# Performance work log

Measured on AMD Instinct MI355X. Metric: run time of the kernel, lower is better.

The kernel has to match this reference:

```python
import jax, jax.numpy as jnp
from jax import lax
import numpy as np

N, L = 32, 2048
TABLES, INPUT_SIZE, DEM_IN, DEM_OUT = 4, 1024, 8, 20
C_TAB = INPUT_SIZE // TABLES  # 256
LIN_IN = INPUT_SIZE + DEM_OUT  # 1044
EPS = 1e-5


def _layernorm(x):
    # LNNormalizer modeled as affine-free LayerNorm over last dim
    mu = jnp.mean(x, axis=-1, keepdims=True)
    var = jnp.mean(jnp.square(x - mu), axis=-1, keepdims=True)
    return (x - mu) * lax.rsqrt(var + EPS)


def setup_inputs() -> dict:
    key = jax.random.key(0)
    ks = jax.random.split(key, 11)
    inp = {
        "dem": jax.random.normal(ks[0], (N, DEM_IN), jnp.float32),
        "ts0": jax.random.normal(ks[1], (N, L, C_TAB), jnp.float32),
        "ts1": jax.random.normal(ks[2], (N, L, C_TAB), jnp.float32),
        "ts2": jax.random.normal(ks[3], (N, L, C_TAB), jnp.float32),
        "ts3": jax.random.normal(ks[4], (N, L, C_TAB), jnp.float32),
        "W_dem1": jax.random.normal(ks[5], (DEM_IN, 40), jnp.float32) * (1.0 / np.sqrt(DEM_IN)),
        "b_dem1": jnp.zeros((40,), jnp.float32),
        "W_dem2": jax.random.normal(ks[6], (40, DEM_OUT), jnp.float32) * (1.0 / np.sqrt(40.0)),
        "b_dem2": jnp.zeros((DEM_OUT,), jnp.float32),
        "W_lin": jax.random.normal(ks[7], (LIN_IN, C_TAB), jnp.float32) * (1.0 / np.sqrt(LIN_IN)),
        "b_lin": jnp.zeros((C_TAB,), jnp.float32),
    }
    return inp


def reference(dem, ts0, ts1, ts2, ts3, W_dem1, b_dem1, W_dem2, b_dem2, W_lin, b_lin):
    # dem_fc: 8 -> 40 -> 20 with ReLUs (dropout=0)
    d = jax.nn.relu(dem @ W_dem1 + b_dem1)
    d = jax.nn.relu(d @ W_dem2 + b_dem2)                 # [N, 20]
    dem_exp = jnp.broadcast_to(d[:, None, :], (N, L, DEM_OUT))

    x = jnp.concatenate([ts0, ts1, ts2, ts3, dem_exp], axis=-1)  # [N, L, 1044]
    x = x @ W_lin + b_lin                                        # [N, L, 256]

    t = jnp.arange(L, dtype=jnp.int32)[None, :, None]            # [1, L, 1]
    pad_mask = t < (L - 1)  # positions whose causal window includes zero padding

    # --- causal max pool (= cummax, with padding zeros in window) + argmax ---
    idx = jnp.broadcast_to(t, x.shape).astype(jnp.int32)

    def comb(a, b):
        va, ia = a
        vb, ib = b
        keep = va >= vb  # first-occurrence tie-break, like torch max_pool1d
        return jnp.where(keep, va, vb), jnp.where(keep, ia, ib)

    cmax, carg = lax.associative_scan(comb, (x, idx), axis=1)
    p_max = jnp.where(pad_mask, jnp.maximum(cmax, 0.0), cmax)    # [N, L, 256]
    # torch index into padded buffer minus (L-1): padding zero (at window start,
    time_inds = jnp.where(pad_mask & (cmax <= 0.0), t - (L - 1), carg)

    # --- causal avg pool: window always L, zeros counted (count_include_pad) ---
    csum = jnp.cumsum(x, axis=1)
    p_avg = csum / jnp.float32(L)

    # --- norm_sum_pool1d: causal sum normalized by sqrt(#valid elements) ---
    p_sum = csum * lax.rsqrt((t + 1).astype(jnp.float32))

    activations = jnp.swapaxes(p_max, 1, 2)      # [N, C, L], pre-normalization
    time_inds_out = jnp.swapaxes(time_inds, 1, 2)

    p_max = _layernorm(p_max)
    p_avg = _layernorm(p_avg)
    p_sum = _layernorm(p_sum)

    out = jnp.concatenate([p_max, p_avg, p_sum, dem_exp], axis=-1)  # [N, L, 788]
    return out, time_inds_out, activations
```

## Files before the change

kernel.cpp:

```cpp
#include <hip/hip_runtime.h>

#define NBATCH 32
#define LSEQ   2048
#define CDIM   256
#define KDIM   1024
#define DEMI   8
#define H1DIM  40
#define DEMO   20
#define NCHUNK 32
#define CHLEN  64
#define LNEPS  1e-5f

#define OFF_X    0L
#define OFF_S    16777216L
#define OFF_AGM  33554432L
#define OFF_AGS  33816576L
#define OFF_AGI  34078720L
#define OFF_PRM  34340864L
#define OFF_PRS  34603008L
#define OFF_PRI  34865152L
#define OFF_DV   35127296L
#define OFF_BASE 35127936L

#define OUT0_OFF   0L
#define OUTTI_OFF  51642368L
#define OUTACT_OFF 68419584L

typedef short          s16x8 __attribute__((ext_vector_type(8)));
typedef unsigned short us4   __attribute__((ext_vector_type(4)));
typedef float          f32x4 __attribute__((ext_vector_type(4)));

static __device__ __forceinline__ unsigned short f2bf(float x) {
    unsigned u = __builtin_bit_cast(unsigned, x);
    u += 0x7fffu + ((u >> 16) & 1u);
    return (unsigned short)(u >> 16);
}
static __device__ __forceinline__ float bf2f(unsigned short h) {
    return __builtin_bit_cast(float, ((unsigned)h) << 16);
}

__global__ __launch_bounds__(256) void k_dem(
    const float* __restrict__ dem,
    const float* __restrict__ W1, const float* __restrict__ b1,
    const float* __restrict__ W2, const float* __restrict__ b2,
    const float* __restrict__ Wl, const float* __restrict__ bl,
    float* __restrict__ dvals, float* __restrict__ base)
{
    __shared__ float h1[NBATCH][H1DIM];
    __shared__ float dsh[NBATCH][DEMO];
    int tid = threadIdx.x;

    for (int idx = tid; idx < NBATCH * H1DIM; idx += 256) {
        int n = idx / H1DIM, o = idx % H1DIM;
        float s = b1[o];
        #pragma unroll
        for (int k = 0; k < DEMI; ++k) s += dem[n * DEMI + k] * W1[k * H1DIM + o];
        h1[n][o] = fmaxf(s, 0.0f);
    }
    __syncthreads();
    for (int idx = tid; idx < NBATCH * DEMO; idx += 256) {
        int n = idx / DEMO, o = idx % DEMO;
        float s = b2[o];
        #pragma unroll
        for (int k = 0; k < H1DIM; ++k) s += h1[n][k] * W2[k * DEMO + o];
        float dv = fmaxf(s, 0.0f);
        dsh[n][o] = dv;
        dvals[idx] = dv;
    }
    __syncthreads();
    for (int idx = tid; idx < NBATCH * CDIM; idx += 256) {
        int n = idx >> 8, c = idx & 255;
        float s = bl[c];
        #pragma unroll
        for (int k = 0; k < DEMO; ++k) s += dsh[n][k] * Wl[(KDIM + k) * CDIM + c];
        base[idx] = s;
    }
}

__global__ __launch_bounds__(256) void k_wconv(
    const float* __restrict__ W, unsigned short* __restrict__ Wf)
{
    int idx = blockIdx.x * 256 + threadIdx.x;
    int k = idx >> 8, c = idx & 255;
    float w = W[idx];
    unsigned short h = f2bf(w);
    float r1 = w - bf2f(h);
    unsigned short m = f2bf(r1);
    float r2 = r1 - bf2f(m);
    unsigned short l = f2bf(r2);
    int kstep = k >> 5;
    int nt = c >> 4;
    int ln = (c & 15) + (((k & 31) >> 3) << 4);
    int e = k & 7;
    long o = (((long)(kstep * 3) * 16 + nt) * 64 + ln) * 8 + e;
    Wf[o]         = h;
    Wf[o + 8192]  = m;
    Wf[o + 16384] = l;
}

__global__ __launch_bounds__(256) void k_gemm(
    const float* __restrict__ ts0, const float* __restrict__ ts1,
    const float* __restrict__ ts2, const float* __restrict__ ts3,
    const unsigned short* __restrict__ Wf, const float* __restrict__ base,
    float* __restrict__ X)
{
    __shared__ unsigned short Af[3][8][64][8];
    __shared__ unsigned short Bf[3][8][64][8];

    const int tid  = threadIdx.x;
    const int lane = tid & 63;
    const int wid  = tid >> 6;

    const int mb = blockIdx.x >> 1;
    const int cb = (blockIdx.x & 1) << 7;
    const int n  = mb >> 4;
    const int t0 = (mb & 15) << 7;

    const int kq  = tid & 1;
    const int am  = tid >> 1;
    const int amt = am >> 4, aml = am & 15;
    const long arow = ((long)(n * LSEQ + t0 + am)) * CDIM;

    f32x4 acc[4][4];
    #pragma unroll
    for (int i = 0; i < 4; ++i)
        #pragma unroll
        for (int j = 0; j < 4; ++j)
            #pragma unroll
            for (int r = 0; r < 4; ++r) acc[i][j][r] = 0.0f;

    const uint4* wsrc = (const uint4*)Wf;
    uint4* bdst = (uint4*)(&Bf[0][0][0][0]);

    for (int k0 = 0; k0 < KDIM; k0 += 32) {
        const float* tsp = (k0 < 256) ? ts0 : (k0 < 512) ? ts1 : (k0 < 768) ? ts2 : ts3;
        const int joff = k0 & 255;

        float4 av[4];
        #pragma unroll
        for (int j = 0; j < 4; ++j)
            av[j] = *(const float4*)(tsp + arow + joff + kq * 4 + j * 8);

        const int kstep = k0 >> 5;
        const long wbase = (long)kstep * 3072 + ((cb >> 4) << 6);
        uint4 bv[6];
        #pragma unroll
        for (int p = 0; p < 3; ++p) {
            bv[p * 2 + 0] = wsrc[wbase + p * 1024 + tid];
            bv[p * 2 + 1] = wsrc[wbase + p * 1024 + tid + 256];
        }

        __syncthreads();

        #pragma unroll
        for (int j = 0; j < 4; ++j) {
            const float vv[4] = {av[j].x, av[j].y, av[j].z, av[j].w};
            us4 hv, mv, lv;
            #pragma unroll
            for (int q = 0; q < 4; ++q) {
                float v = vv[q];
                unsigned short h = f2bf(v);
                float r1 = v - bf2f(h);
                unsigned short m = f2bf(r1);
                float r2 = r1 - bf2f(m);
                unsigned short l = f2bf(r2);
                hv[q] = h; mv[q] = m; lv[q] = l;
            }
            const int ln = aml + (j << 4);
            const int e0 = kq << 2;
            *(us4*)&Af[0][amt][ln][e0] = hv;
            *(us4*)&Af[1][amt][ln][e0] = mv;
            *(us4*)&Af[2][amt][ln][e0] = lv;
        }
        #pragma unroll
        for (int p = 0; p < 3; ++p) {
            bdst[p * 512 + tid]       = bv[p * 2 + 0];
            bdst[p * 512 + tid + 256] = bv[p * 2 + 1];
        }

        __syncthreads();

        const int wmt = (wid >> 1) << 2;
        const int wnt = (wid & 1) << 2;
        s16x8 ah[4], am2[4], al2[4];
        #pragma unroll
        for (int mt = 0; mt < 4; ++mt) {
            ah[mt]  = *(const s16x8*)&Af[0][wmt + mt][lane][0];
            am2[mt] = *(const s16x8*)&Af[1][wmt + mt][lane][0];
            al2[mt] = *(const s16x8*)&Af[2][wmt + mt][lane][0];
        }
        #pragma unroll
        for (int nt = 0; nt < 4; ++nt) {
            s16x8 bh = *(const s16x8*)&Bf[0][wnt + nt][lane][0];
            s16x8 bm = *(const s16x8*)&Bf[1][wnt + nt][lane][0];
            s16x8 bl = *(const s16x8*)&Bf[2][wnt + nt][lane][0];
            #pragma unroll
            for (int mt = 0; mt < 4; ++mt) {
                acc[mt][nt] = __builtin_amdgcn_mfma_f32_16x16x32_bf16(ah[mt],  bl, acc[mt][nt], 0, 0, 0);
                acc[mt][nt] = __builtin_amdgcn_mfma_f32_16x16x32_bf16(al2[mt], bh, acc[mt][nt], 0, 0, 0);
                acc[mt][nt] = __builtin_amdgcn_mfma_f32_16x16x32_bf16(am2[mt], bm, acc[mt][nt], 0, 0, 0);
                acc[mt][nt] = __builtin_amdgcn_mfma_f32_16x16x32_bf16(ah[mt],  bm, acc[mt][nt], 0, 0, 0);
                acc[mt][nt] = __builtin_amdgcn_mfma_f32_16x16x32_bf16(am2[mt], bh, acc[mt][nt], 0, 0, 0);
                acc[mt][nt] = __builtin_amdgcn_mfma_f32_16x16x32_bf16(ah[mt],  bh, acc[mt][nt], 0, 0, 0);
            }
        }
    }

    const int rb = ((wid >> 1) << 6) + ((lane >> 4) << 2);
    const int cc = cb + ((wid & 1) << 6) + (lane & 15);
    float bb[4];
    #pragma unroll
    for (int nt = 0; nt < 4; ++nt) bb[nt] = base[n * CDIM + cc + nt * 16];

    #pragma unroll
    for (int mt = 0; mt < 4; ++mt) {
        #pragma unroll
        for (int r = 0; r < 4; ++r) {
            long off = ((long)(n * LSEQ) + t0 + rb + mt * 16 + r) * CDIM + cc;
            #pragma unroll
            for (int nt = 0; nt < 4; ++nt)
                X[off + nt * 16] = acc[mt][nt][r] + bb[nt];
        }
    }
}

__global__ __launch_bounds__(256) void k_agg(
    const float* __restrict__ X,
    float* __restrict__ agm, float* __restrict__ ags, int* __restrict__ agi)
{
    int c = threadIdx.x;
    int n = blockIdx.x >> 5, ch = blockIdx.x & 31;
    int t0 = ch * CHLEN;
    const float* p = X + ((long)n * LSEQ + t0) * CDIM + c;
    float vm = -3.4e38f; int im = t0; float sm = 0.0f;
    #pragma unroll 4
    for (int tt = 0; tt < CHLEN; ++tt) {
        float v = p[(long)tt * CDIM];
        if (v > vm) { vm = v; im = t0 + tt; }
        sm += v;
    }
    int o = (n * NCHUNK + ch) * CDIM + c;
    agm[o] = vm; ags[o] = sm; agi[o] = im;
}

__global__ __launch_bounds__(256) void k_pre(
    const float* __restrict__ agm, const float* __restrict__ ags, const int* __restrict__ agi,
    float* __restrict__ prm, float* __restrict__ prs, int* __restrict__ pri)
{
    int c = threadIdx.x;
    int n = blockIdx.x;
    float vm = -3.4e38f; int im = 0; float sm = 0.0f;
    for (int ch = 0; ch < NCHUNK; ++ch) {
        int o = (n * NCHUNK + ch) * CDIM + c;
        prm[o] = vm; pri[o] = im; prs[o] = sm;
        float av = agm[o]; float as = ags[o]; int ai = agi[o];
        if (av > vm) { vm = av; im = ai; }
        sm += as;
    }
}

__global__ __launch_bounds__(256) void k_scan(
    float* __restrict__ X, float* __restrict__ S,
    const float* __restrict__ prm, const float* __restrict__ prs, const int* __restrict__ pri,
    float* __restrict__ Ttmp)
{
    int c = threadIdx.x;
    int n = blockIdx.x >> 5, ch = blockIdx.x & 31;
    int t0 = ch * CHLEN;
    int o = (n * NCHUNK + ch) * CDIM + c;
    float vm = prm[o]; int im = pri[o]; float sm = prs[o];
    long rb = ((long)n * LSEQ + t0) * CDIM + c;
    #pragma unroll 4
    for (int tt = 0; tt < CHLEN; ++tt) {
        int t = t0 + tt;
        long idx = rb + (long)tt * CDIM;
        float v = X[idx];
        if (v > vm) { vm = v; im = t; }
        sm += v;
        bool pad = t < (LSEQ - 1);
        float pm = pad ? fmaxf(vm, 0.0f) : vm;
        int ti = (pad && vm <= 0.0f) ? (t - (LSEQ - 1)) : im;
        X[idx] = pm;
        S[idx] = sm;
        Ttmp[idx] = (float)ti;
    }
}

__global__ __launch_bounds__(256) void k_tr(
    const float* __restrict__ src, float* __restrict__ dst)
{
    __shared__ float tile[64][65];
    int n  = blockIdx.z;
    int tB = blockIdx.x;
    int cB = blockIdx.y;
    int tid = threadIdx.x;
    int i0 = tid >> 4;
    int j4 = tid & 15;

    const float* sp = src + ((long)n * LSEQ + tB * 64) * CDIM + cB * 64;
    #pragma unroll
    for (int r = 0; r < 4; ++r) {
        int i = i0 + r * 16;
        float4 v = *(const float4*)(sp + (long)i * CDIM + j4 * 4);
        tile[i][j4 * 4 + 0] = v.x;
        tile[i][j4 * 4 + 1] = v.y;
        tile[i][j4 * 4 + 2] = v.z;
        tile[i][j4 * 4 + 3] = v.w;
    }
    __syncthreads();
    float* dp = dst + ((long)n * CDIM + cB * 64) * LSEQ + tB * 64;
    #pragma unroll
    for (int r = 0; r < 4; ++r) {
        int j = i0 + r * 16;
        float4 v;
        v.x = tile[j4 * 4 + 0][j];
        v.y = tile[j4 * 4 + 1][j];
        v.z = tile[j4 * 4 + 2][j];
        v.w = tile[j4 * 4 + 3][j];
        *(float4*)(dp + (long)j * LSEQ + j4 * 4) = v;
    }
}

__global__ __launch_bounds__(256) void k_ln(
    const float* __restrict__ P, const float* __restrict__ S,
    const float* __restrict__ dvals, float* __restrict__ out0)
{
    int tid = threadIdx.x;
    int wid = tid >> 6, lane = tid & 63;
    long row = (long)blockIdx.x * 4 + wid;
    int n = (int)(row >> 11);
    int t = (int)(row & 2047);
    long ib = row * CDIM + lane * 4;

    float4 p = *(const float4*)(P + ib);
    float4 s = *(const float4*)(S + ib);

    float sum_p = p.x + p.y + p.z + p.w;
    float sq_p  = p.x * p.x + p.y * p.y + p.z * p.z + p.w * p.w;
    float sum_s = s.x + s.y + s.z + s.w;
    float sq_s  = s.x * s.x + s.y * s.y + s.z * s.z + s.w * s.w;

    #pragma unroll
    for (int off = 32; off > 0; off >>= 1) {
        sum_p += __shfl_xor(sum_p, off);
        sq_p  += __shfl_xor(sq_p, off);
        sum_s += __shfl_xor(sum_s, off);
        sq_s  += __shfl_xor(sq_s, off);
    }

    const float inv = 1.0f / 256.0f;
    float mu_p = sum_p * inv;
    float var_p = sq_p * inv - mu_p * mu_p;
    float mu_s = sum_s * inv;
    float var_s = sq_s * inv - mu_s * mu_s;

    float r1 = 1.0f / sqrtf(var_p + LNEPS);
    const float a = 1.0f / 2048.0f;
    float r2 = a / sqrtf(a * a * var_s + LNEPS);
    float b = 1.0f / sqrtf((float)(t + 1));
    float r3 = b / sqrtf(b * b * var_s + LNEPS);

    float* ob = out0 + row * 788;
    float4 o1 = {(p.x - mu_p) * r1, (p.y - mu_p) * r1, (p.z - mu_p) * r1, (p.w - mu_p) * r1};
    *(float4*)(ob + lane * 4) = o1;
    float4 o2 = {(s.x - mu_s) * r2, (s.y - mu_s) * r2, (s.z - mu_s) * r2, (s.w - mu_s) * r2};
    *(float4*)(ob + 256 + lane * 4) = o2;
    float4 o3 = {(s.x - mu_s) * r3, (s.y - mu_s) * r3, (s.z - mu_s) * r3, (s.w - mu_s) * r3};
    *(float4*)(ob + 512 + lane * 4) = o3;
    if (lane < 5) {
        float4 dv = *(const float4*)(dvals + n * DEMO + lane * 4);
        *(float4*)(ob + 768 + lane * 4) = dv;
    }
}

extern "C" void kernel_launch(void* const* d_in, const int* in_sizes, int n_in,
                              void* d_out, int out_size, void* d_ws, size_t ws_size,
                              hipStream_t stream)
{
    const float* dem = (const float*)d_in[0];
    const float* ts0 = (const float*)d_in[1];
    const float* ts1 = (const float*)d_in[2];
    const float* ts2 = (const float*)d_in[3];
    const float* ts3 = (const float*)d_in[4];
    const float* W1  = (const float*)d_in[5];
    const float* b1  = (const float*)d_in[6];
    const float* W2  = (const float*)d_in[7];
    const float* b2  = (const float*)d_in[8];
    const float* Wl  = (const float*)d_in[9];
    const float* bl  = (const float*)d_in[10];

    float* ws = (float*)d_ws;
    float* X    = ws + OFF_X;
    float* S    = ws + OFF_S;
    float* agm  = ws + OFF_AGM;
    float* ags  = ws + OFF_AGS;
    int*   agi  = (int*)(ws + OFF_AGI);
    float* prm  = ws + OFF_PRM;
    float* prs  = ws + OFF_PRS;
    int*   pri  = (int*)(ws + OFF_PRI);
    float* dv   = ws + OFF_DV;
    float* base = ws + OFF_BASE;
    unsigned short* Wf = (unsigned short*)(ws + OFF_AGM);

    float* out    = (float*)d_out;
    float* outTI  = out + OUTTI_OFF;
    float* outACT = out + OUTACT_OFF;

    k_dem<<<1, 256, 0, stream>>>(dem, W1, b1, W2, b2, Wl, bl, dv, base);
    k_wconv<<<1024, 256, 0, stream>>>(Wl, Wf);
    k_gemm<<<1024, 256, 0, stream>>>(ts0, ts1, ts2, ts3, Wf, base, X);
    k_agg<<<NBATCH * NCHUNK, 256, 0, stream>>>(X, agm, ags, agi);
    k_pre<<<NBATCH, 256, 0, stream>>>(agm, ags, agi, prm, prs, pri);
    k_scan<<<NBATCH * NCHUNK, 256, 0, stream>>>(X, S, prm, prs, pri, outACT);
    k_tr<<<dim3(32, 4, 32), 256, 0, stream>>>(outACT, outTI);
    k_tr<<<dim3(32, 4, 32), 256, 0, stream>>>(X, outACT);
    k_ln<<<16384, 256, 0, stream>>>(X, S, dv, out);
}
```

Baseline: 919.1 us.

## Fuse weight-conversion into dem kernel, prefetch A in GEMM, merge transposes

Merges the weight split-conversion and the dem MLP into one launch. In the GEMM it remaps block indices so neighbouring blocks spread across XCDs, and prefetches the next K-slice of activations into registers while the MFMAs run, moving the barrier to the end of the loop. It also fuses the two transposes into one kernel, staging the time indices in the out0 region so outACT is no longer used as scratch. This cuts launch count and one full pass of global traffic, in exchange for more registers and LDS per block.

```diff
diff --git a/kernel.cpp b/kernel.cpp
--- a/kernel.cpp
+++ b/kernel.cpp
@@ -39,30 +39,49 @@
     return __builtin_bit_cast(float, ((unsigned)h) << 16);
 }
 
-__global__ __launch_bounds__(256) void k_dem(
+__global__ __launch_bounds__(256) void k_demwc(
     const float* __restrict__ dem,
     const float* __restrict__ W1, const float* __restrict__ b1,
     const float* __restrict__ W2, const float* __restrict__ b2,
     const float* __restrict__ Wl, const float* __restrict__ bl,
-    float* __restrict__ dvals, float* __restrict__ base)
-{
-    __shared__ float h1[NBATCH][H1DIM];
+    float* __restrict__ dvals, float* __restrict__ base,
+    unsigned short* __restrict__ Wf)
+{
+    int tid = threadIdx.x;
+    if (blockIdx.x < 1024) {
+        int idx = blockIdx.x * 256 + tid;
+        int k = idx >> 8, c = idx & 255;
+        float w = Wl[idx];
+        unsigned short h = f2bf(w);
+        float r1 = w - bf2f(h);
+        unsigned short m = f2bf(r1);
+        float r2 = r1 - bf2f(m);
+        unsigned short l = f2bf(r2);
+        int kstep = k >> 5;
+        int nt = c >> 4;
+        int ln = (c & 15) + (((k & 31) >> 3) << 4);
+        int e = k & 7;
+        long o = (((long)(kstep * 3) * 16 + nt) * 64 + ln) * 8 + e;
+        Wf[o]         = h;
+        Wf[o + 8192]  = m;
+        Wf[o + 16384] = l;
+        return;
+    }
+    __shared__ float h1s[NBATCH][H1DIM];
     __shared__ float dsh[NBATCH][DEMO];
-    int tid = threadIdx.x;
-
     for (int idx = tid; idx < NBATCH * H1DIM; idx += 256) {
         int n = idx / H1DIM, o = idx % H1DIM;
         float s = b1[o];
         #pragma unroll
         for (int k = 0; k < DEMI; ++k) s += dem[n * DEMI + k] * W1[k * H1DIM + o];
-        h1[n][o] = fmaxf(s, 0.0f);
+        h1s[n][o] = fmaxf(s, 0.0f);
     }
     __syncthreads();
     for (int idx = tid; idx < NBATCH * DEMO; idx += 256) {
         int n = idx / DEMO, o = idx % DEMO;
         float s = b2[o];
         #pragma unroll
-        for (int k = 0; k < H1DIM; ++k) s += h1[n][k] * W2[k * DEMO + o];
+        for (int k = 0; k < H1DIM; ++k) s += h1s[n][k] * W2[k * DEMO + o];
         float dv = fmaxf(s, 0.0f);
         dsh[n][o] = dv;
         dvals[idx] = dv;
@@ -75,27 +94,6 @@
         for (int k = 0; k < DEMO; ++k) s += dsh[n][k] * Wl[(KDIM + k) * CDIM + c];
         base[idx] = s;
     }
-}
-
-__global__ __launch_bounds__(256) void k_wconv(
-    const float* __restrict__ W, unsigned short* __restrict__ Wf)
-{
-    int idx = blockIdx.x * 256 + threadIdx.x;
-    int k = idx >> 8, c = idx & 255;
-    float w = W[idx];
-    unsigned short h = f2bf(w);
-    float r1 = w - bf2f(h);
-    unsigned short m = f2bf(r1);
-    float r2 = r1 - bf2f(m);
-    unsigned short l = f2bf(r2);
-    int kstep = k >> 5;
-    int nt = c >> 4;
-    int ln = (c & 15) + (((k & 31) >> 3) << 4);
-    int e = k & 7;
-    long o = (((long)(kstep * 3) * 16 + nt) * 64 + ln) * 8 + e;
-    Wf[o]         = h;
-    Wf[o + 8192]  = m;
-    Wf[o + 16384] = l;
 }
 
 __global__ __launch_bounds__(256) void k_gemm(
@@ -111,8 +109,10 @@
     const int lane = tid & 63;
     const int wid  = tid >> 6;
 
-    const int mb = blockIdx.x >> 1;
-    const int cb = (blockIdx.x & 1) << 7;
+    const int bid     = blockIdx.x;
+    const int logical = (bid & 7) * 128 + (bid >> 3);
+    const int mb = logical >> 1;
+    const int cb = (logical & 1) << 7;
     const int n  = mb >> 4;
     const int t0 = (mb & 15) << 7;
 
@@ -132,15 +132,12 @@
     const uint4* wsrc = (const uint4*)Wf;
     uint4* bdst = (uint4*)(&Bf[0][0][0][0]);
 
+    float4 av[4];
+    #pragma unroll
+    for (int j = 0; j < 4; ++j)
+        av[j] = *(const float4*)(ts0 + arow + kq * 4 + j * 8);
+
     for (int k0 = 0; k0 < KDIM; k0 += 32) {
-        const float* tsp = (k0 < 256) ? ts0 : (k0 < 512) ? ts1 : (k0 < 768) ? ts2 : ts3;
-        const int joff = k0 & 255;
-
-        float4 av[4];
-        #pragma unroll
-        for (int j = 0; j < 4; ++j)
-            av[j] = *(const float4*)(tsp + arow + joff + kq * 4 + j * 8);
-
         const int kstep = k0 >> 5;
         const long wbase = (long)kstep * 3072 + ((cb >> 4) << 6);
         uint4 bv[6];
@@ -149,8 +146,6 @@
             bv[p * 2 + 0] = wsrc[wbase + p * 1024 + tid];
             bv[p * 2 + 1] = wsrc[wbase + p * 1024 + tid + 256];
         }
-
-        __syncthreads();
 
         #pragma unroll
         for (int j = 0; j < 4; ++j) {
@@ -175,10 +170,19 @@
         #pragma unroll
         for (int p = 0; p < 3; ++p) {
             bdst[p * 512 + tid]       = bv[p * 2 + 0];
-            bdst[p * 512 + tid + 256] = bv[p * 2 + 1];
+            bdst[p * 512 + 256 + tid] = bv[p * 2 + 1];
         }
 
         __syncthreads();
+
+        if (k0 + 32 < KDIM) {
+            const int k1 = k0 + 32;
+            const float* tspn = (k1 < 256) ? ts0 : (k1 < 512) ? ts1 : (k1 < 768) ? ts2 : ts3;
+            const int joffn = k1 & 255;
+            #pragma unroll
+            for (int j = 0; j < 4; ++j)
+                av[j] = *(const float4*)(tspn + arow + joffn + kq * 4 + j * 8);
+        }
 
         const int wmt = (wid >> 1) << 2;
         const int wnt = (wid & 1) << 2;
@@ -204,6 +208,8 @@
                 acc[mt][nt] = __builtin_amdgcn_mfma_f32_16x16x32_bf16(ah[mt],  bh, acc[mt][nt], 0, 0, 0);
             }
         }
+
+        __syncthreads();
     }
 
     const int rb = ((wid >> 1) << 6) + ((lane >> 4) << 2);
@@ -286,10 +292,12 @@
     }
 }
 
-__global__ __launch_bounds__(256) void k_tr(
-    const float* __restrict__ src, float* __restrict__ dst)
-{
-    __shared__ float tile[64][65];
+__global__ __launch_bounds__(256) void k_tr2(
+    const float* __restrict__ srcT, float* __restrict__ dstT,
+    const float* __restrict__ srcX, float* __restrict__ dstX)
+{
+    __shared__ float tileT[64][65];
+    __shared__ float tileX[64][65];
     int n  = blockIdx.z;
     int tB = blockIdx.x;
     int cB = blockIdx.y;
@@ -297,27 +305,29 @@
     int i0 = tid >> 4;
     int j4 = tid & 15;
 
-    const float* sp = src + ((long)n * LSEQ + tB * 64) * CDIM + cB * 64;
+    long sbase = ((long)n * LSEQ + tB * 64) * CDIM + cB * 64;
     #pragma unroll
     for (int r = 0; r < 4; ++r) {
         int i = i0 + r * 16;
-        float4 v = *(const float4*)(sp + (long)i * CDIM + j4 * 4);
-        tile[i][j4 * 4 + 0] = v.x;
-        tile[i][j4 * 4 + 1] = v.y;
-        tile[i][j4 * 4 + 2] = v.z;
-        tile[i][j4 * 4 + 3] = v.w;
+        float4 vT = *(const float4*)(srcT + sbase + (long)i * CDIM + j4 * 4);
+        float4 vX = *(const float4*)(srcX + sbase + (long)i * CDIM + j4 * 4);
+        tileT[i][j4 * 4 + 0] = vT.x; tileT[i][j4 * 4 + 1] = vT.y;
+        tileT[i][j4 * 4 + 2] = vT.z; tileT[i][j4 * 4 + 3] = vT.w;
+        tileX[i][j4 * 4 + 0] = vX.x; tileX[i][j4 * 4 + 1] = vX.y;
+        tileX[i][j4 * 4 + 2] = vX.z; tileX[i][j4 * 4 + 3] = vX.w;
     }
     __syncthreads();
-    float* dp = dst + ((long)n * CDIM + cB * 64) * LSEQ + tB * 64;
+    long dbase = ((long)n * CDIM + cB * 64) * LSEQ + tB * 64;
     #pragma unroll
     for (int r = 0; r < 4; ++r) {
         int j = i0 + r * 16;
-        float4 v;
-        v.x = tile[j4 * 4 + 0][j];
-        v.y = tile[j4 * 4 + 1][j];
-        v.z = tile[j4 * 4 + 2][j];
-        v.w = tile[j4 * 4 + 3][j];
-        *(float4*)(dp + (long)j * LSEQ + j4 * 4) = v;
+        float4 vT, vX;
+        vT.x = tileT[j4 * 4 + 0][j]; vT.y = tileT[j4 * 4 + 1][j];
+        vT.z = tileT[j4 * 4 + 2][j]; vT.w = tileT[j4 * 4 + 3][j];
+        vX.x = tileX[j4 * 4 + 0][j]; vX.y = tileX[j4 * 4 + 1][j];
+        vX.z = tileX[j4 * 4 + 2][j]; vX.w = tileX[j4 * 4 + 3][j];
+        *(float4*)(dstT + dbase + (long)j * LSEQ + j4 * 4) = vT;
+        *(float4*)(dstX + dbase + (long)j * LSEQ + j4 * 4) = vX;
     }
 }
 
@@ -405,14 +415,13 @@
     float* out    = (float*)d_out;
     float* outTI  = out + OUTTI_OFF;
     float* outACT = out + OUTACT_OFF;
-
-    k_dem<<<1, 256, 0, stream>>>(dem, W1, b1, W2, b2, Wl, bl, dv, base);
-    k_wconv<<<1024, 256, 0, stream>>>(Wl, Wf);
+    float* Ttmp   = out + OUT0_OFF;
+
+    k_demwc<<<1025, 256, 0, stream>>>(dem, W1, b1, W2, b2, Wl, bl, dv, base, Wf);
     k_gemm<<<1024, 256, 0, stream>>>(ts0, ts1, ts2, ts3, Wf, base, X);
     k_agg<<<NBATCH * NCHUNK, 256, 0, stream>>>(X, agm, ags, agi);
     k_pre<<<NBATCH, 256, 0, stream>>>(agm, ags, agi, prm, prs, pri);
-    k_scan<<<NBATCH * NCHUNK, 256, 0, stream>>>(X, S, prm, prs, pri, outACT);
-    k_tr<<<dim3(32, 4, 32), 256, 0, stream>>>(outACT, outTI);
-    k_tr<<<dim3(32, 4, 32), 256, 0, stream>>>(X, outACT);
+    k_scan<<<NBATCH * NCHUNK, 256, 0, stream>>>(X, S, prm, prs, pri, Ttmp);
+    k_tr2<<<dim3(32, 4, 32), 256, 0, stream>>>(Ttmp, outTI, X, outACT);
     k_ln<<<16384, 256, 0, stream>>>(X, S, dv, out);
 }
```

New measurement: 753.5 us. -18.0%, faster.
